# Optimization experiments

Hardware: AMD Instinct MI355X
Metric: run time of the kernel (lower is better)

## Reference

```python
import jax, jax.numpy as jnp
import numpy as np

N = 50000      # nodes
E = 1600000    # edges per graph
IN = 64
HID = 64
OUT = 64


def _gat_conv(x, edge_index, W, a_src, a_dst, bias):
    """PyG GATConv, heads=1, add_self_loops=True, negative_slope=0.2."""
    n = x.shape[0]
    h = x @ W                                   # [N, d]
    loop = jnp.arange(n, dtype=edge_index.dtype)
    src = jnp.concatenate([edge_index[0], loop])
    dst = jnp.concatenate([edge_index[1], loop])
    e = jax.nn.leaky_relu((h @ a_src)[src] + (h @ a_dst)[dst], negative_slope=0.2)
    m = jax.ops.segment_max(e, dst, num_segments=n)          # stable edge-softmax per dst
    w = jnp.exp(e - m[dst])
    denom = jax.ops.segment_sum(w, dst, num_segments=n)
    alpha = w / denom[dst]                                   # [E+N]
    out = jax.ops.segment_sum(h[src] * alpha[:, None], dst, num_segments=n)
    return out + bias


def setup_inputs() -> dict:
    key = jax.random.key(0)
    ks = jax.random.split(key, 32)

    def glorot(k, shape):
        fan_out = shape[1] if len(shape) > 1 else 1
        lim = (6.0 / (shape[0] + fan_out)) ** 0.5
        return jax.random.uniform(k, shape, minval=-lim, maxval=lim, dtype=jnp.float32)

    inp = {
        "x_ind": jax.random.normal(ks[0], (N, IN), jnp.float32),
        "x_pos": jax.random.normal(ks[1], (N, IN), jnp.float32),
        "edge_ind": jax.random.randint(ks[2], (2, E), 0, N, dtype=jnp.int32),
        "edge_pos": jax.random.randint(ks[3], (2, E), 0, N, dtype=jnp.int32),
        "w1_ind": glorot(ks[4], (IN, HID)),
        "as1_ind": glorot(ks[5], (HID,)),
        "ad1_ind": glorot(ks[6], (HID,)),
        "b1_ind": jnp.zeros((HID,), jnp.float32),
        "w2_ind": glorot(ks[7], (HID, OUT)),
        "as2_ind": glorot(ks[8], (OUT,)),
        "ad2_ind": glorot(ks[9], (OUT,)),
        "b2_ind": jnp.zeros((OUT,), jnp.float32),
        "w1_pos": glorot(ks[10], (IN, HID)),
        "as1_pos": glorot(ks[11], (HID,)),
        "ad1_pos": glorot(ks[12], (HID,)),
        "b1_pos": jnp.zeros((HID,), jnp.float32),
        "w2_pos": glorot(ks[13], (HID, OUT)),
        "as2_pos": glorot(ks[14], (OUT,)),
        "ad2_pos": glorot(ks[15], (OUT,)),
        "b2_pos": jnp.zeros((OUT,), jnp.float32),
        "first_hop_att": glorot(ks[16], (2, HID)),
        "att_weight": glorot(ks[17], (2, OUT)),
        "mlp_w": glorot(ks[18], (OUT, 1)),
        "mlp_b": jnp.zeros((1,), jnp.float32),
    }
    return inp


def reference(x_ind, x_pos, edge_ind, edge_pos,
              w1_ind, as1_ind, ad1_ind, b1_ind,
              w2_ind, as2_ind, ad2_ind, b2_ind,
              w1_pos, as1_pos, ad1_pos, b1_pos,
              w2_pos, as2_pos, ad2_pos, b2_pos,
              first_hop_att, att_weight, mlp_w, mlp_b):
    h_i = jax.nn.relu(_gat_conv(x_ind, edge_ind, w1_ind, as1_ind, ad1_ind, b1_ind))
    h_p = jax.nn.relu(_gat_conv(x_pos, edge_pos, w1_pos, as1_pos, ad1_pos, b1_pos))
    # first-hop branch attention over the two graphs
    s1 = jnp.stack([jnp.sum(first_hop_att[0] * h_i, axis=1),
                    jnp.sum(first_hop_att[1] * h_p, axis=1)], axis=0)  # [2, N]
    a1 = jax.nn.softmax(s1, axis=0)
    fused = a1[0][:, None] * h_i + a1[1][:, None] * h_p
    g_i = _gat_conv(fused, edge_ind, w2_ind, as2_ind, ad2_ind, b2_ind)
    g_p = _gat_conv(fused, edge_pos, w2_pos, as2_pos, ad2_pos, b2_pos)
    s2 = jnp.stack([jnp.sum(att_weight[0] * g_i, axis=1),
                    jnp.sum(att_weight[1] * g_p, axis=1)], axis=0)
    a2 = jax.nn.softmax(s2, axis=0)
    x = a2[0][:, None] * g_i + a2[1][:, None] * g_p
    return x @ mlp_w + mlp_b                    # [N, 1]
```

## Files before the change

kernel.cpp:

```cpp
#include <hip/hip_runtime.h>
#include <hip/hip_fp16.h>

#define ND 64
#define BG 256
#define MAXB 512
#define PCH 16384
#define CAP 9216

__device__ __forceinline__ float lrelu(float x) { return x > 0.f ? x : 0.2f * x; }

__device__ __forceinline__ float wave_sum(float v) {
#pragma unroll
    for (int m = 32; m > 0; m >>= 1) v += __shfl_xor(v, m, 64);
    return v;
}

__device__ __forceinline__ void fma8(float* acc, float w, int4 raw) {
    union { int4 i; __half h[8]; } u;
    u.i = raw;
#pragma unroll
    for (int i = 0; i < 8; i++) acc[i] = fmaf(w, __half2float(u.h[i]), acc[i]);
}


__global__ void init_cursor(int* __restrict__ bcursor, int nb) {
    int t = threadIdx.x;
    if (t < nb) bcursor[t] = t * CAP;
}

__device__ void partition_body(int* hist, int* lcur,
                               const int* __restrict__ eI, const int* __restrict__ eP,
                               int* __restrict__ bcursor, int* __restrict__ part,
                               int N, int E, int nb) {
    int t = threadIdx.x;
    int total = 2 * E;
    int chunkBase = blockIdx.x * PCH;
    int cnt = min(PCH, total - chunkBase);
    if (t < nb) hist[t] = 0;
    __syncthreads();

    if (cnt == PCH) {
        int pk[16];
        unsigned bkp[8];
#pragma unroll
        for (int it = 0; it < 4; it++) {
            int i = t * 4 + it * 4096;
            int e = chunkBase + i;
            int sv[4], dv[4];
            if (e + 3 < E) {
                int4 a = *(const int4*)(eI + e);
                int4 b = *(const int4*)(eI + E + e);
                sv[0] = a.x; sv[1] = a.y; sv[2] = a.z; sv[3] = a.w;
                dv[0] = b.x; dv[1] = b.y; dv[2] = b.z; dv[3] = b.w;
            } else if (e >= E) {
                int4 a = *(const int4*)(eP + (e - E));
                int4 b = *(const int4*)(eP + E + (e - E));
                sv[0] = a.x; sv[1] = a.y; sv[2] = a.z; sv[3] = a.w;
                dv[0] = b.x + N; dv[1] = b.y + N; dv[2] = b.z + N; dv[3] = b.w + N;
            } else {
#pragma unroll
                for (int k = 0; k < 4; k++) {
                    int ee = e + k;
                    if (ee < E) { sv[k] = eI[ee]; dv[k] = eI[E + ee]; }
                    else        { sv[k] = eP[ee - E]; dv[k] = N + eP[E + ee - E]; }
                }
            }
#pragma unroll
            for (int k = 0; k < 4; k++) {
                int j = it * 4 + k;
                int bk = dv[k] >> 8;
                pk[j] = (sv[k] << 8) | (dv[k] & 255);
                atomicAdd(&hist[bk], 1);
                if ((j & 1) == 0) bkp[j >> 1] = (unsigned)bk;
                else bkp[j >> 1] |= (unsigned)bk << 16;
            }
        }
        __syncthreads();
        if (t < nb) lcur[t] = hist[t] ? atomicAdd(&bcursor[t], hist[t]) : 0;
        __syncthreads();
#pragma unroll
        for (int j = 0; j < 16; j++) {
            int bk = (bkp[j >> 1] >> ((j & 1) * 16)) & 0xffff;
            int pos = atomicAdd(&lcur[bk], 1);
            part[pos] = pk[j];
        }
        return;
    }

    int cnt4 = cnt & ~3;
    for (int i = t * 4; i < cnt4; i += 4096) {
        int e = chunkBase + i;
        int4 d; int base;
        if (e + 3 < E)   { d = *(const int4*)(eI + E + e); base = 0; }
        else if (e >= E) { d = *(const int4*)(eP + E + (e - E)); base = N; }
        else {
            int tmp[4];
#pragma unroll
            for (int k = 0; k < 4; k++) {
                int ee = e + k;
                tmp[k] = (ee < E) ? eI[E + ee] : N + eP[E + ee - E];
            }
            d = make_int4(tmp[0], tmp[1], tmp[2], tmp[3]); base = 0;
        }
        atomicAdd(&hist[(base + d.x) >> 8], 1);
        atomicAdd(&hist[(base + d.y) >> 8], 1);
        atomicAdd(&hist[(base + d.z) >> 8], 1);
        atomicAdd(&hist[(base + d.w) >> 8], 1);
    }
    for (int i = cnt4 + t; i < cnt; i += 1024) {
        int e = chunkBase + i;
        int idx = (e < E) ? eI[E + e] : N + eP[E + (e - E)];
        atomicAdd(&hist[idx >> 8], 1);
    }
    __syncthreads();
    if (t < nb) lcur[t] = hist[t] ? atomicAdd(&bcursor[t], hist[t]) : 0;
    __syncthreads();
    for (int i = t; i < cnt; i += 1024) {
        int e = chunkBase + i;
        int s, idx;
        if (e < E) { s = eI[e]; idx = eI[E + e]; }
        else       { s = eP[e - E]; idx = N + eP[E + (e - E)]; }
        int pos = atomicAdd(&lcur[idx >> 8], 1);
        part[pos] = (s << 8) | (idx & 255);
    }
}

__device__ void gemm_body(float* xsAll, int gb,
                          const float* __restrict__ xA, const float* __restrict__ xB,
                          const float* __restrict__ WA, const float* __restrict__ WB,
                          const float* __restrict__ asA, const float* __restrict__ adA,
                          const float* __restrict__ asB, const float* __restrict__ adB,
                          __half* __restrict__ h16, float* __restrict__ ssrc,
                          float* __restrict__ sdst, int N) {
    int half = gb & 1;
    int blk = gb >> 1;
    int wave = threadIdx.x >> 6;
    int lane = threadIdx.x & 63;
    const float* x  = half ? xB : xA;
    const float* W  = half ? WB : WA;
    const float* av_ = half ? asB : asA;
    const float* dv_ = half ? adB : adA;
    int nodeBase = (blk * 16 + wave) * 4;
    float* xs = xsAll + wave * (4 * ND);

    if (nodeBase + 3 < N) {
        *(float4*)&xs[lane * 4] = *(const float4*)&x[(size_t)nodeBase * ND + lane * 4];
    } else if (nodeBase < N) {
#pragma unroll
        for (int i = 0; i < 4; i++) {
            int gi = nodeBase * ND + lane * 4 + i;
            xs[lane * 4 + i] = (gi < N * ND) ? x[gi] : 0.f;
        }
    }
    __syncthreads();
    if (nodeBase >= N) return;

    float4 acc = {0.f, 0.f, 0.f, 0.f};
#pragma unroll
    for (int k = 0; k < ND; k++) {
        float wv = W[k * ND + lane];
        acc.x = fmaf(xs[0 * ND + k], wv, acc.x);
        acc.y = fmaf(xs[1 * ND + k], wv, acc.y);
        acc.z = fmaf(xs[2 * ND + k], wv, acc.z);
        acc.w = fmaf(xs[3 * ND + k], wv, acc.w);
    }
    float av = av_[lane], dv = dv_[lane];
    float s1x = wave_sum(acc.x * av), s2x = wave_sum(acc.x * dv);
    float s1y = wave_sum(acc.y * av), s2y = wave_sum(acc.y * dv);
    float s1z = wave_sum(acc.z * av), s2z = wave_sum(acc.z * dv);
    float s1w = wave_sum(acc.w * av), s2w = wave_sum(acc.w * dv);

    int g0 = half * N + nodeBase;
    h16[(size_t)(g0 + 0) * ND + lane] = __float2half(acc.x);
    if (nodeBase + 1 < N) h16[(size_t)(g0 + 1) * ND + lane] = __float2half(acc.y);
    if (nodeBase + 2 < N) h16[(size_t)(g0 + 2) * ND + lane] = __float2half(acc.z);
    if (nodeBase + 3 < N) h16[(size_t)(g0 + 3) * ND + lane] = __float2half(acc.w);
    if (lane == 0) {
        ssrc[g0] = s1x; sdst[g0] = s2x;
        if (nodeBase + 1 < N) { ssrc[g0 + 1] = s1y; sdst[g0 + 1] = s2y; }
        if (nodeBase + 2 < N) { ssrc[g0 + 2] = s1z; sdst[g0 + 2] = s2z; }
        if (nodeBase + 3 < N) { ssrc[g0 + 3] = s1w; sdst[g0 + 3] = s2w; }
    }
}

__global__ void __launch_bounds__(1024) part_gemm(
        const int* __restrict__ eI, const int* __restrict__ eP,
        int* __restrict__ bcursor, int* __restrict__ part,
        const float* __restrict__ xA, const float* __restrict__ xB,
        const float* __restrict__ WA, const float* __restrict__ WB,
        const float* __restrict__ asA, const float* __restrict__ adA,
        const float* __restrict__ asB, const float* __restrict__ adB,
        __half* __restrict__ h16, float* __restrict__ ssrc, float* __restrict__ sdst,
        int N, int E, int nb, int partBlocks) {
    __shared__ int smem[16 * 4 * ND];
    if (blockIdx.x < partBlocks) {
        partition_body(smem, smem + MAXB, eI, eP, bcursor, part, N, E, nb);
    } else {
        gemm_body((float*)smem, blockIdx.x - partBlocks,
                  xA, xB, WA, WB, asA, adA, asB, adB, h16, ssrc, sdst, N);
    }
}

__global__ void bucket_build(const int* __restrict__ part, const int* __restrict__ bcursor,
                             int* __restrict__ row, int* __restrict__ deg,
                             int* __restrict__ csr, int n2, int N) {
    __shared__ int lhist[BG * 4];
    __shared__ int lrow[BG * 4];
    __shared__ int slab[CAP];
    int b = blockIdx.x, t = threadIdx.x;
    int start = b * CAP;
    int cnt = min(bcursor[b] - start, CAP);
    int cnt4 = cnt & ~3;
    int q1 = N >> 2, q2 = N >> 1, q3 = q1 + q2;
    auto key = [&](int p) {
        int s = p >> 8;
        int q = (s >= q2) ? 2 : 0;
        q += (s >= (q ? q3 : q1)) ? 1 : 0;
        return ((p & 255) << 2) | q;
    };
    lhist[t] = 0;
    __syncthreads();
    for (int j = t * 4; j < cnt4; j += 4096) {
        int4 p = *(const int4*)(part + start + j);
        atomicAdd(&lhist[key(p.x)], 1);
        atomicAdd(&lhist[key(p.y)], 1);
        atomicAdd(&lhist[key(p.z)], 1);
        atomicAdd(&lhist[key(p.w)], 1);
    }
    for (int j = cnt4 + t; j < cnt; j += 1024) atomicAdd(&lhist[key(part[start + j])], 1);
    __syncthreads();
    int v = lhist[t];
    lrow[t] = v;
    __syncthreads();
    for (int off = 1; off < 1024; off <<= 1) {
        int a = (t >= off) ? lrow[t - off] : 0;
        __syncthreads();
        lrow[t] += a;
        __syncthreads();
    }
    if (t < BG) {
        int g = b * BG + t;
        if (g < n2) {
            row[g] = start + lrow[4 * t] - lhist[4 * t];
            deg[g] = lhist[4 * t] + lhist[4 * t + 1] + lhist[4 * t + 2] + lhist[4 * t + 3];
        }
    }
    __syncthreads();
    lhist[t] = lrow[t] - v;
    __syncthreads();
    for (int j = t * 4; j < cnt4; j += 4096) {
        int4 p = *(const int4*)(part + start + j);
        int pos;
        pos = atomicAdd(&lhist[key(p.x)], 1); slab[pos] = p.x >> 8;
        pos = atomicAdd(&lhist[key(p.y)], 1); slab[pos] = p.y >> 8;
        pos = atomicAdd(&lhist[key(p.z)], 1); slab[pos] = p.z >> 8;
        pos = atomicAdd(&lhist[key(p.w)], 1); slab[pos] = p.w >> 8;
    }
    for (int j = cnt4 + t; j < cnt; j += 1024) {
        int p = part[start + j];
        int pos = atomicAdd(&lhist[key(p)], 1);
        slab[pos] = p >> 8;
    }
    __syncthreads();
    {
        int ge = lrow[t], gs = ge - v;
        for (int i = gs + 1; i < ge; i++) {
            int x = slab[i], j2 = i - 1;
            while (j2 >= gs && slab[j2] > x) { slab[j2 + 1] = slab[j2]; j2--; }
            slab[j2 + 1] = x;
        }
    }
    __syncthreads();
    for (int j = t; j < cnt; j += 1024) csr[start + j] = slab[j];
}

__global__ void gemm2_fused(const float* __restrict__ hbig, const float* __restrict__ fha,
                            const float* __restrict__ WA, const float* __restrict__ WB,
                            const float* __restrict__ asA, const float* __restrict__ adA,
                            const float* __restrict__ asB, const float* __restrict__ adB,
                            __half* __restrict__ h16, float* __restrict__ ssrc,
                            float* __restrict__ sdst, int N) {
    __shared__ float xs[4][4 * ND];
    int half = blockIdx.x & 1;
    int blk = blockIdx.x >> 1;
    int wave = threadIdx.x >> 6;
    int lane = threadIdx.x & 63;
    const float* W  = half ? WB : WA;
    const float* av_ = half ? asB : asA;
    const float* dv_ = half ? adB : adA;
    int nodeBase = (blk * 4 + wave) * 4;
    float* xsw = xs[wave];

    if (nodeBase < N) {
        int nd = nodeBase + (lane >> 4);
        int col = (lane & 15) * 4;
        float4 vi = *(const float4*)&hbig[(size_t)nd * ND + col];
        float4 vp = *(const float4*)&hbig[((size_t)N + nd) * ND + col];
        float4 a0 = *(const float4*)&fha[col];
        float4 a1 = *(const float4*)&fha[ND + col];
        float p0 = vi.x * a0.x + vi.y * a0.y + vi.z * a0.z + vi.w * a0.w;
        float p1 = vp.x * a1.x + vp.y * a1.y + vp.z * a1.z + vp.w * a1.w;
#pragma unroll
        for (int m = 1; m <= 8; m <<= 1) {
            p0 += __shfl_xor(p0, m, 64);
            p1 += __shfl_xor(p1, m, 64);
        }
        float mx = fmaxf(p0, p1);
        float e0 = __expf(p0 - mx), e1 = __expf(p1 - mx);
        float inv = 1.f / (e0 + e1);
        float4 f;
        f.x = (e0 * vi.x + e1 * vp.x) * inv;
        f.y = (e0 * vi.y + e1 * vp.y) * inv;
        f.z = (e0 * vi.z + e1 * vp.z) * inv;
        f.w = (e0 * vi.w + e1 * vp.w) * inv;
        *(float4*)&xsw[lane * 4] = f;
    }
    __syncthreads();
    if (nodeBase >= N) return;

    float4 acc = {0.f, 0.f, 0.f, 0.f};
#pragma unroll
    for (int k = 0; k < ND; k++) {
        float wv = W[k * ND + lane];
        acc.x = fmaf(xsw[0 * ND + k], wv, acc.x);
        acc.y = fmaf(xsw[1 * ND + k], wv, acc.y);
        acc.z = fmaf(xsw[2 * ND + k], wv, acc.z);
        acc.w = fmaf(xsw[3 * ND + k], wv, acc.w);
    }
    float av = av_[lane], dv = dv_[lane];
    float s1x = wave_sum(acc.x * av), s2x = wave_sum(acc.x * dv);
    float s1y = wave_sum(acc.y * av), s2y = wave_sum(acc.y * dv);
    float s1z = wave_sum(acc.z * av), s2z = wave_sum(acc.z * dv);
    float s1w = wave_sum(acc.w * av), s2w = wave_sum(acc.w * dv);

    int g0 = half * N + nodeBase;
    h16[(size_t)(g0 + 0) * ND + lane] = __float2half(acc.x);
    h16[(size_t)(g0 + 1) * ND + lane] = __float2half(acc.y);
    h16[(size_t)(g0 + 2) * ND + lane] = __float2half(acc.z);
    h16[(size_t)(g0 + 3) * ND + lane] = __float2half(acc.w);
    if (lane == 0) {
        ssrc[g0] = s1x; sdst[g0] = s2x;
        ssrc[g0 + 1] = s1y; sdst[g0 + 1] = s2y;
        ssrc[g0 + 2] = s1z; sdst[g0 + 2] = s2z;
        ssrc[g0 + 3] = s1w; sdst[g0 + 3] = s2w;
    }
}

__global__ void aggregate_dual(const int* __restrict__ csr, const int* __restrict__ row,
                               const int* __restrict__ deg, const float* __restrict__ ssrc,
                               const float* __restrict__ sdst, const __half* __restrict__ h16,
                               const float* __restrict__ bA, const float* __restrict__ bB,
                               float* __restrict__ out, int N, int relu) {
    int half = blockIdx.x & 1;
    int wave = threadIdx.x >> 6;
    int lane = threadIdx.x & 63;
    int sub  = lane >> 4;
    int l16  = lane & 15;
    int slot = l16 >> 3;
    int fl8  = (l16 & 7) * 8;
    int node = ((blockIdx.x >> 1) * 4 + wave) * 4 + sub;
    bool valid = node < N;
    int g = half * N + node;
    const float* bias = half ? bB : bA;
    const float* ss = ssrc + (size_t)half * N;
    const __half* hh = h16 + (size_t)half * N * ND;

    int start = valid ? row[g] : 0;
    int cnt   = valid ? deg[g] : 0;
    float sd  = valid ? sdst[g] : 0.f;
    float wself = valid ? __expf(lrelu(ss[node] + sd)) : 0.f;

    float acc[8] = {0.f, 0.f, 0.f, 0.f, 0.f, 0.f, 0.f, 0.f};
    float denomp = 0.f;
    int waveBase = sub << 4;

    int c16 = min(16, cnt);
    int sj = (l16 < c16) ? csr[start + l16] : 0;
    float wj = (l16 < c16) ? __expf(lrelu(ss[sj] + sd)) : 0.f;

    for (int base = 0; base < cnt; base += 16) {
        int nb2 = base + 16;
        int sjn = 0; float svn = 0.f; int c16n = cnt - nb2;
        if (nb2 < cnt) {
            sjn = (l16 < c16n) ? csr[start + nb2 + l16] : 0;
            svn = (l16 < c16n) ? ss[sjn] : 0.f;
        }
        denomp += wj;
        int nq = (min(16, cnt - base) + 1) >> 1;
        float w0 = __shfl(wj, waveBase + slot, 64);
        int s0 = __shfl(sj, waveBase + slot, 64);
        int4 r0 = *(const int4*)(hh + (size_t)s0 * ND + fl8);
        if (nq > 1) {
            float w1 = __shfl(wj, waveBase + 2 + slot, 64);
            int s1 = __shfl(sj, waveBase + 2 + slot, 64);
            int4 r1 = *(const int4*)(hh + (size_t)s1 * ND + fl8);
            for (int c = 2; c < nq; c++) {
                float w2 = __shfl(wj, waveBase + c * 2 + slot, 64);
                int s2 = __shfl(sj, waveBase + c * 2 + slot, 64);
                int4 r2 = *(const int4*)(hh + (size_t)s2 * ND + fl8);
                fma8(acc, w0, r0);
                w0 = w1; r0 = r1;
                w1 = w2; r1 = r2;
            }
            fma8(acc, w0, r0);
            fma8(acc, w1, r1);
        } else {
            fma8(acc, w0, r0);
        }
        if (nb2 < cnt) {
            wj = (l16 < c16n) ? __expf(lrelu(svn + sd)) : 0.f;
            sj = sjn;
        }
    }

#pragma unroll
    for (int i = 0; i < 8; i++) acc[i] += __shfl_xor(acc[i], 8, 64);
#pragma unroll
    for (int m = 1; m <= 8; m <<= 1) denomp += __shfl_xor(denomp, m, 64);
    float denom = denomp + wself;

    if (!valid || slot != 0) return;
    int4 rawS = *(const int4*)(hh + (size_t)node * ND + fl8);
    union { int4 i; __half h[8]; } us;
    us.i = rawS;
    float v[8];
#pragma unroll
    for (int i = 0; i < 8; i++)
        v[i] = (acc[i] + wself * __half2float(us.h[i])) / denom + bias[fl8 + i];
    if (relu) {
#pragma unroll
        for (int i = 0; i < 8; i++) v[i] = fmaxf(v[i], 0.f);
    }
    *(float4*)&out[(size_t)g * ND + fl8]     = make_float4(v[0], v[1], v[2], v[3]);
    *(float4*)&out[(size_t)g * ND + fl8 + 4] = make_float4(v[4], v[5], v[6], v[7]);
}

__global__ void branch_att_mlp(const float* __restrict__ hbig, const float* __restrict__ att,
                               const float* __restrict__ mlpw, const float* __restrict__ mlpb,
                               float* __restrict__ out, int n) {
    int gid = blockIdx.x * blockDim.x + threadIdx.x;
    int node = gid >> 6, lane = gid & 63;
    if (node >= n) return;
    float vi = hbig[(size_t)node * ND + lane];
    float vp = hbig[((size_t)n + node) * ND + lane];
    float s0 = wave_sum(att[lane] * vi);
    float s1 = wave_sum(att[ND + lane] * vp);
    float m = fmaxf(s0, s1);
    float a0 = __expf(s0 - m), a1 = __expf(s1 - m);
    float xj = (a0 * vi + a1 * vp) / (a0 + a1);
    float o = wave_sum(xj * mlpw[lane]);
    if (lane == 0) out[node] = o + mlpb[0];
}

extern "C" void kernel_launch(void* const* d_in, const int* in_sizes, int n_in,
                              void* d_out, int out_size, void* d_ws, size_t ws_size,
                              hipStream_t stream) {
    const int N = in_sizes[0] / ND;
    const int E = in_sizes[2] / 2;

    const float* x_ind = (const float*)d_in[0];
    const float* x_pos = (const float*)d_in[1];
    const int*   e_ind = (const int*)d_in[2];
    const int*   e_pos = (const int*)d_in[3];
    const float* w1i = (const float*)d_in[4];
    const float* as1i = (const float*)d_in[5];
    const float* ad1i = (const float*)d_in[6];
    const float* b1i = (const float*)d_in[7];
    const float* w2i = (const float*)d_in[8];
    const float* as2i = (const float*)d_in[9];
    const float* ad2i = (const float*)d_in[10];
    const float* b2i = (const float*)d_in[11];
    const float* w1p = (const float*)d_in[12];
    const float* as1p = (const float*)d_in[13];
    const float* ad1p = (const float*)d_in[14];
    const float* b1p = (const float*)d_in[15];
    const float* w2p = (const float*)d_in[16];
    const float* as2p = (const float*)d_in[17];
    const float* ad2p = (const float*)d_in[18];
    const float* b2p = (const float*)d_in[19];
    const float* fha = (const float*)d_in[20];
    const float* attw = (const float*)d_in[21];
    const float* mlpw = (const float*)d_in[22];
    const float* mlpb = (const float*)d_in[23];

    char* ws = (char*)d_ws;
    size_t off = 0;
    auto alloc = [&](size_t elems) { void* p = ws + off; off += elems * 4; return p; };

    const int n2 = 2 * N;
    const int nb = (n2 + BG - 1) / BG;

    __half* h16 = (__half*)alloc((size_t)n2 * ND / 2);
    float* hbig = (float*)alloc((size_t)n2 * ND);
    float* ssrc = (float*)alloc(n2);
    float* sdst = (float*)alloc(n2);
    int* deg    = (int*)alloc(n2);
    int* rowi   = (int*)alloc(n2);
    int* csr    = (int*)alloc((size_t)nb * CAP);
    int* bcursor= (int*)alloc(MAXB);
    int* part   = (int*)hbig;

    const int partBlocks  = (2 * E + PCH - 1) / PCH;
    const int gemm1Blocks = 2 * ((N + 63) / 64);
    const int gemm2Blocks = 2 * ((N + 15) / 16);
    const int aggBlocks   = 2 * ((N + 15) / 16);
    const int nodeBlocks  = (N + 3) / 4;

    init_cursor<<<1, 512, 0, stream>>>(bcursor, nb);
    part_gemm<<<partBlocks + gemm1Blocks, 1024, 0, stream>>>(
        e_ind, e_pos, bcursor, part,
        x_ind, x_pos, w1i, w1p, as1i, ad1i, as1p, ad1p,
        h16, ssrc, sdst, N, E, nb, partBlocks);
    bucket_build<<<nb, 1024, 0, stream>>>(part, bcursor, rowi, deg, csr, n2, N);

    aggregate_dual<<<aggBlocks, 256, 0, stream>>>(csr, rowi, deg, ssrc, sdst, h16,
                                                  b1i, b1p, hbig, N, 1);

    gemm2_fused<<<gemm2Blocks, 256, 0, stream>>>(hbig, fha, w2i, w2p,
                                                 as2i, ad2i, as2p, ad2p,
                                                 h16, ssrc, sdst, N);
    aggregate_dual<<<aggBlocks, 256, 0, stream>>>(csr, rowi, deg, ssrc, sdst, h16,
                                                  b2i, b2p, hbig, N, 0);
    branch_att_mlp<<<nodeBlocks, 256, 0, stream>>>(hbig, attw, mlpw, mlpb,
                                                   (float*)d_out, N);
}
```

Baseline: 344.6 us.

## Halve destination bucket size and widen aggregation edge batches to 32

Destination buckets shrink from 256 to 128 nodes, doubling the bucket count and giving bucket_build an 8-way source-range subsort instead of 4-way, which is meant to improve locality of neighbour feature gathers. The aggregation loop now prefetches two 16-edge groups per iteration and keeps a three-deep pipeline of gathered feature rows to hide memory latency. This adds register pressure and more buckets and launch blocks. The packed part encoding still keeps the low 8 destination bits, although only 7 are now used.

```diff
diff --git a/kernel.cpp b/kernel.cpp
--- a/kernel.cpp
+++ b/kernel.cpp
@@ -2,10 +2,10 @@
 #include <hip/hip_fp16.h>
 
 #define ND 64
-#define BG 256
-#define MAXB 512
+#define BG 128
+#define MAXB 1024
 #define PCH 16384
-#define CAP 9216
+#define CAP 4608
 
 __device__ __forceinline__ float lrelu(float x) { return x > 0.f ? x : 0.2f * x; }
 
@@ -68,7 +68,7 @@
 #pragma unroll
             for (int k = 0; k < 4; k++) {
                 int j = it * 4 + k;
-                int bk = dv[k] >> 8;
+                int bk = dv[k] >> 7;
                 pk[j] = (sv[k] << 8) | (dv[k] & 255);
                 atomicAdd(&hist[bk], 1);
                 if ((j & 1) == 0) bkp[j >> 1] = (unsigned)bk;
@@ -102,15 +102,15 @@
             }
             d = make_int4(tmp[0], tmp[1], tmp[2], tmp[3]); base = 0;
         }
-        atomicAdd(&hist[(base + d.x) >> 8], 1);
-        atomicAdd(&hist[(base + d.y) >> 8], 1);
-        atomicAdd(&hist[(base + d.z) >> 8], 1);
-        atomicAdd(&hist[(base + d.w) >> 8], 1);
+        atomicAdd(&hist[(base + d.x) >> 7], 1);
+        atomicAdd(&hist[(base + d.y) >> 7], 1);
+        atomicAdd(&hist[(base + d.z) >> 7], 1);
+        atomicAdd(&hist[(base + d.w) >> 7], 1);
     }
     for (int i = cnt4 + t; i < cnt; i += 1024) {
         int e = chunkBase + i;
         int idx = (e < E) ? eI[E + e] : N + eP[E + (e - E)];
-        atomicAdd(&hist[idx >> 8], 1);
+        atomicAdd(&hist[idx >> 7], 1);
     }
     __syncthreads();
     if (t < nb) lcur[t] = hist[t] ? atomicAdd(&bcursor[t], hist[t]) : 0;
@@ -120,7 +120,7 @@
         int s, idx;
         if (e < E) { s = eI[e]; idx = eI[E + e]; }
         else       { s = eP[e - E]; idx = N + eP[E + (e - E)]; }
-        int pos = atomicAdd(&lcur[idx >> 8], 1);
+        int pos = atomicAdd(&lcur[idx >> 7], 1);
         part[pos] = (s << 8) | (idx & 255);
     }
 }
@@ -204,19 +204,20 @@
 __global__ void bucket_build(const int* __restrict__ part, const int* __restrict__ bcursor,
                              int* __restrict__ row, int* __restrict__ deg,
                              int* __restrict__ csr, int n2, int N) {
-    __shared__ int lhist[BG * 4];
-    __shared__ int lrow[BG * 4];
+    __shared__ int lhist[BG * 8];
+    __shared__ int lrow[BG * 8];
     __shared__ int slab[CAP];
     int b = blockIdx.x, t = threadIdx.x;
     int start = b * CAP;
     int cnt = min(bcursor[b] - start, CAP);
     int cnt4 = cnt & ~3;
-    int q1 = N >> 2, q2 = N >> 1, q3 = q1 + q2;
+    int t1 = (N * 1) >> 3, t2 = (N * 2) >> 3, t3 = (N * 3) >> 3, t4 = (N * 4) >> 3;
+    int t5 = (N * 5) >> 3, t6 = (N * 6) >> 3, t7 = (N * 7) >> 3;
     auto key = [&](int p) {
         int s = p >> 8;
-        int q = (s >= q2) ? 2 : 0;
-        q += (s >= (q ? q3 : q1)) ? 1 : 0;
-        return ((p & 255) << 2) | q;
+        int o = (s >= t1) + (s >= t2) + (s >= t3) + (s >= t4)
+              + (s >= t5) + (s >= t6) + (s >= t7);
+        return ((p & 127) << 3) | o;
     };
     lhist[t] = 0;
     __syncthreads();
@@ -241,8 +242,11 @@
     if (t < BG) {
         int g = b * BG + t;
         if (g < n2) {
-            row[g] = start + lrow[4 * t] - lhist[4 * t];
-            deg[g] = lhist[4 * t] + lhist[4 * t + 1] + lhist[4 * t + 2] + lhist[4 * t + 3];
+            row[g] = start + lrow[8 * t] - lhist[8 * t];
+            int d = 0;
+#pragma unroll
+            for (int i = 0; i < 8; i++) d += lhist[8 * t + i];
+            deg[g] = d;
         }
     }
     __syncthreads();
@@ -374,42 +378,64 @@
     float denomp = 0.f;
     int waveBase = sub << 4;
 
-    int c16 = min(16, cnt);
-    int sj = (l16 < c16) ? csr[start + l16] : 0;
-    float wj = (l16 < c16) ? __expf(lrelu(ss[sj] + sd)) : 0.f;
-
-    for (int base = 0; base < cnt; base += 16) {
-        int nb2 = base + 16;
-        int sjn = 0; float svn = 0.f; int c16n = cnt - nb2;
+    int c0 = min(16, cnt), c1 = min(16, cnt - 16);
+    int sj0 = (l16 < c0) ? csr[start + l16] : 0;
+    int sj1 = (l16 < c1) ? csr[start + 16 + l16] : 0;
+    float wj0 = (l16 < c0) ? __expf(lrelu(ss[sj0] + sd)) : 0.f;
+    float wj1 = (l16 < c1) ? __expf(lrelu(ss[sj1] + sd)) : 0.f;
+
+    auto fetchW = [&](int c, float& w, int& s) {
+        float wv = (c >= 8) ? wj1 : wj0;
+        int   sv = (c >= 8) ? sj1 : sj0;
+        int e = 2 * c + slot;
+        int sl = waveBase + (e & 15);
+        w = __shfl(wv, sl, 64);
+        s = __shfl(sv, sl, 64);
+    };
+
+    for (int base = 0; base < cnt; base += 32) {
+        int nb2 = base + 32;
+        int sn0 = 0, sn1 = 0; float v0 = 0.f, v1 = 0.f;
+        int d0 = cnt - nb2, d1 = cnt - nb2 - 16;
         if (nb2 < cnt) {
-            sjn = (l16 < c16n) ? csr[start + nb2 + l16] : 0;
-            svn = (l16 < c16n) ? ss[sjn] : 0.f;
-        }
-        denomp += wj;
-        int nq = (min(16, cnt - base) + 1) >> 1;
-        float w0 = __shfl(wj, waveBase + slot, 64);
-        int s0 = __shfl(sj, waveBase + slot, 64);
+            sn0 = (l16 < d0) ? csr[start + nb2 + l16] : 0;
+            v0  = (l16 < d0) ? ss[sn0] : 0.f;
+            sn1 = (l16 < d1) ? csr[start + nb2 + 16 + l16] : 0;
+            v1  = (l16 < d1) ? ss[sn1] : 0.f;
+        }
+        denomp += wj0 + wj1;
+        int nq = (min(32, cnt - base) + 1) >> 1;
+        float w0, w1, w2; int s0, s1, s2;
+        fetchW(0, w0, s0);
         int4 r0 = *(const int4*)(hh + (size_t)s0 * ND + fl8);
-        if (nq > 1) {
-            float w1 = __shfl(wj, waveBase + 2 + slot, 64);
-            int s1 = __shfl(sj, waveBase + 2 + slot, 64);
+        if (nq > 2) {
+            fetchW(1, w1, s1);
             int4 r1 = *(const int4*)(hh + (size_t)s1 * ND + fl8);
-            for (int c = 2; c < nq; c++) {
-                float w2 = __shfl(wj, waveBase + c * 2 + slot, 64);
-                int s2 = __shfl(sj, waveBase + c * 2 + slot, 64);
-                int4 r2 = *(const int4*)(hh + (size_t)s2 * ND + fl8);
+            fetchW(2, w2, s2);
+            int4 r2 = *(const int4*)(hh + (size_t)s2 * ND + fl8);
+            for (int c = 3; c < nq; c++) {
+                float w3; int s3;
+                fetchW(c, w3, s3);
+                int4 r3 = *(const int4*)(hh + (size_t)s3 * ND + fl8);
                 fma8(acc, w0, r0);
                 w0 = w1; r0 = r1;
                 w1 = w2; r1 = r2;
+                w2 = w3; r2 = r3;
             }
+            fma8(acc, w0, r0);
+            fma8(acc, w1, r1);
+            fma8(acc, w2, r2);
+        } else if (nq == 2) {
+            fetchW(1, w1, s1);
+            int4 r1 = *(const int4*)(hh + (size_t)s1 * ND + fl8);
             fma8(acc, w0, r0);
             fma8(acc, w1, r1);
         } else {
             fma8(acc, w0, r0);
         }
         if (nb2 < cnt) {
-            wj = (l16 < c16n) ? __expf(lrelu(svn + sd)) : 0.f;
-            sj = sjn;
+            wj0 = (l16 < d0) ? __expf(lrelu(v0 + sd)) : 0.f; sj0 = sn0;
+            wj1 = (l16 < d1) ? __expf(lrelu(v1 + sd)) : 0.f; sj1 = sn1;
         }
     }
 
@@ -506,7 +532,7 @@
     const int aggBlocks   = 2 * ((N + 15) / 16);
     const int nodeBlocks  = (N + 3) / 4;
 
-    init_cursor<<<1, 512, 0, stream>>>(bcursor, nb);
+    init_cursor<<<1, 1024, 0, stream>>>(bcursor, nb);
     part_gemm<<<partBlocks + gemm1Blocks, 1024, 0, stream>>>(
         e_ind, e_pos, bcursor, part,
         x_ind, x_pos, w1i, w1p, as1i, ad1i, as1p, ad1p,
```

Result: no change. 343.6 us (-0.3%).
